# Kernel optimization log

Measured on AMD Instinct MI355X. Metric: run time of the kernel, lower is better.

Reference implementation:

```python
import jax, jax.numpy as jnp
import numpy as np

W_BIT = 8

def quantize_weight(w, k=W_BIT):
    # DoReFa-style weight quantization (conv2d_Q_fn): tanh-normalize to [0,1],
    # uniform-quantize to 2^k-1 levels (round with straight-through), map to [-1,1].
    n = float(2 ** k - 1)
    t = jnp.tanh(w)
    t = t / (2.0 * jnp.max(jnp.abs(t))) + 0.5
    q = t + jax.lax.stop_gradient(jnp.round(t * n) / n - t)
    return 2.0 * q - 1.0

def qconv(x, w, b, pad):
    wq = quantize_weight(w)
    y = jax.lax.conv_general_dilated(
        x, wq, window_strides=(1, 1), padding=[(pad, pad), (pad, pad)],
        dimension_numbers=('NCHW', 'OIHW', 'NCHW'))
    return y + b[None, :, None, None]

def upsample2x(x):
    # nearest-neighbor, scale_factor=2
    return jnp.repeat(jnp.repeat(x, 2, axis=2), 2, axis=3)

def setup_inputs() -> dict:
    key = jax.random.key(0)
    ks = jax.random.split(key, 11)
    F = 256
    C3 = jax.random.normal(ks[0], (8, 512, 64, 64), dtype=jnp.float32)
    C4 = jax.random.normal(ks[1], (8, 1024, 32, 32), dtype=jnp.float32)
    C5 = jax.random.normal(ks[2], (8, 2048, 16, 16), dtype=jnp.float32)
    # conv params (torch nn.Conv2d default has bias)
    w5 = jax.random.normal(ks[3], (F, 2048, 1, 1), dtype=jnp.float32) * 0.02
    b5 = jax.random.normal(ks[4], (F,), dtype=jnp.float32) * 0.01
    w4 = jax.random.normal(ks[5], (F, 1024, 1, 1), dtype=jnp.float32) * 0.02
    b4 = jax.random.normal(ks[6], (F,), dtype=jnp.float32) * 0.01
    w3 = jax.random.normal(ks[7], (F, 512, 1, 1), dtype=jnp.float32) * 0.02
    b3 = jax.random.normal(ks[8], (F,), dtype=jnp.float32) * 0.01
    w3_2 = jax.random.normal(ks[9], (F, F, 3, 3), dtype=jnp.float32) * 0.02
    b3_2 = jax.random.normal(ks[10], (F,), dtype=jnp.float32) * 0.01
    return {"C3": C3, "C4": C4, "C5": C5,
            "w5": w5, "b5": b5, "w4": w4, "b4": b4,
            "w3": w3, "b3": b3, "w3_2": w3_2, "b3_2": b3_2}

def reference(C3, C4, C5, w5, b5, w4, b4, w3, b3, w3_2, b3_2):
    P5_x = qconv(C5, w5, b5, pad=0)            # [B,256,16,16]
    P5_up = upsample2x(P5_x)                   # [B,256,32,32]
    P4_x = qconv(C4, w4, b4, pad=0) + P5_up    # [B,256,32,32]
    P4_up = upsample2x(P4_x)                   # [B,256,64,64]
    P3_x = qconv(C3, w3, b3, pad=0) + P4_up    # [B,256,64,64]
    P3_x = qconv(P3_x, w3_2, b3_2, pad=1)      # [B,256,64,64]
    return P3_x
```

## Files before the change

kernel.cpp:

```cpp
#include <hip/hip_runtime.h>
#include <stdint.h>

typedef unsigned short u16;
typedef short s16x8 __attribute__((ext_vector_type(8)));
typedef short s16x4 __attribute__((ext_vector_type(4)));
typedef float f32x4 __attribute__((ext_vector_type(4)));
typedef unsigned int u32x4 __attribute__((ext_vector_type(4)));

__device__ __forceinline__ u16 f2bf(float x) {
    unsigned u = __float_as_uint(x);
    unsigned r = u + 0x7FFFu + ((u >> 16) & 1u);
    return (u16)(r >> 16);
}

__device__ __forceinline__ void gll16(void* lds, const void* g) {
    __builtin_amdgcn_global_load_lds(
        (const __attribute__((address_space(1))) void*)g,
        (__attribute__((address_space(3))) void*)lds,
        16, 0, 0);
}

__global__ __launch_bounds__(256) void reduce_maxabs(
    const float* __restrict__ a0, int n0, const float* __restrict__ a1, int n1,
    const float* __restrict__ a2, int n2, const float* __restrict__ a3, int n3,
    float* __restrict__ out) {
    int which = blockIdx.y;
    const float* w = which == 0 ? a0 : which == 1 ? a1 : which == 2 ? a2 : a3;
    int n = which == 0 ? n0 : which == 1 ? n1 : which == 2 ? n2 : n3;
    float m = 0.f;
    for (int i = blockIdx.x * 256 + threadIdx.x; i < n; i += gridDim.x * 256)
        m = fmaxf(m, fabsf(tanhf(w[i])));
#pragma unroll
    for (int off = 32; off > 0; off >>= 1)
        m = fmaxf(m, __shfl_down(m, off, 64));
    __shared__ float sm[4];
    if ((threadIdx.x & 63) == 0) sm[threadIdx.x >> 6] = m;
    __syncthreads();
    if (threadIdx.x == 0) {
        m = fmaxf(fmaxf(sm[0], sm[1]), fmaxf(sm[2], sm[3]));
        atomicMax((int*)out + which, __float_as_int(m));
    }
}

__global__ __launch_bounds__(256) void quant_weights(
    const float* __restrict__ w5, const float* __restrict__ w4,
    const float* __restrict__ w3, const float* __restrict__ w32,
    const float* __restrict__ mx,
    u16* __restrict__ q5, u16* __restrict__ q4,
    u16* __restrict__ q3, u16* __restrict__ q2) {
    int which = blockIdx.y;
    const float* w = which == 0 ? w5 : which == 1 ? w4 : which == 2 ? w3 : w32;
    int n = which == 0 ? 524288 : which == 1 ? 262144 : which == 2 ? 131072 : 589824;
    int i = blockIdx.x * 256 + threadIdx.x;
    if (i >= n) return;
    float inv = 0.5f / mx[which];
    float t = tanhf(w[i]) * inv + 0.5f;
    float q = rintf(t * 255.f) * (1.f / 255.f);
    u16 o = f2bf(2.f * q - 1.f);
    if (which == 0) q5[i] = o;
    else if (which == 1) q4[i] = o;
    else if (which == 2) q3[i] = o;
    else {
        int kw = i % 3, kh = (i / 3) % 3, c = (i / 9) & 255, f = i / 2304;
        q2[(size_t)((kh * 3 + kw) * 256 + f) * 256 + c] = o;
    }
}

__global__ __launch_bounds__(256) void nchw_to_nhwc_bf16(
    const float* __restrict__ in, u16* __restrict__ outp, int C, int HW) {
    __shared__ float tile[64][65];
    int t = threadIdx.x;
    int hw0 = blockIdx.x << 6, c0 = blockIdx.y << 6, n = blockIdx.z;
    const float* src = in + (size_t)n * C * HW;
#pragma unroll
    for (int j = 0; j < 4; ++j) {
        int c = (t >> 4) + j * 16;
        int hw = (t & 15) << 2;
        f32x4 v = *(const f32x4*)(src + (size_t)(c0 + c) * HW + hw0 + hw);
        tile[c][hw] = v.x; tile[c][hw + 1] = v.y; tile[c][hw + 2] = v.z; tile[c][hw + 3] = v.w;
    }
    __syncthreads();
    u16* dst = outp + (size_t)n * C * HW;
#pragma unroll
    for (int j = 0; j < 16; ++j) {
        int idx = j * 256 + t;
        int c = idx & 63, hw = idx >> 6;
        dst[(size_t)(hw0 + hw) * C + c0 + c] = f2bf(tile[c][hw]);
    }
}

__global__ __launch_bounds__(256) void gemm_qconv(
    const u16* __restrict__ A, const u16* __restrict__ B,
    const float* __restrict__ bias, const float* __restrict__ addsrc,
    float* __restrict__ outF, u16* __restrict__ outB,
    int K, int Wlog, int HWlog) {
    __shared__ u16 As[128 * 64];
    __shared__ u16 Bs[128 * 64];
    int t = threadIdx.x, lane = t & 63, wv = t >> 6;
    int l16 = lane & 15, quad = lane >> 4;
    int f0 = blockIdx.y << 7, p0 = blockIdx.x << 7;
    int wf = (wv >> 1) << 6, wp = (wv & 1) << 6;
    f32x4 acc[4][4] = {};
    const u16* Ab = A + (size_t)f0 * K;
    const u16* Bb = B + (size_t)p0 * K;
    int row = t >> 3, c8 = t & 7;
    for (int k0 = 0; k0 < K; k0 += 64) {
#pragma unroll
        for (int it = 0; it < 4; ++it) {
            gll16(&As[(it * 256 + wv * 64) * 8], Ab + (size_t)(it * 32 + row) * K + k0 + c8 * 8);
            gll16(&Bs[(it * 256 + wv * 64) * 8], Bb + (size_t)(it * 32 + row) * K + k0 + c8 * 8);
        }
        __syncthreads();
#pragma unroll
        for (int kk = 0; kk < 64; kk += 32) {
            s16x8 a[4], b[4];
#pragma unroll
            for (int j = 0; j < 4; ++j)
                a[j] = *(const s16x8*)&As[(wf + 16 * j + l16) * 64 + kk + quad * 8];
#pragma unroll
            for (int i = 0; i < 4; ++i)
                b[i] = *(const s16x8*)&Bs[(wp + 16 * i + l16) * 64 + kk + quad * 8];
#pragma unroll
            for (int j = 0; j < 4; ++j)
#pragma unroll
                for (int i = 0; i < 4; ++i)
                    acc[j][i] = __builtin_amdgcn_mfma_f32_16x16x32_bf16(a[j], b[i], acc[j][i], 0, 0, 0);
        }
        __syncthreads();
    }
    int W = 1 << Wlog;
#pragma unroll
    for (int j = 0; j < 4; ++j) {
        int f = f0 + wf + 16 * j + (quad << 2);
        f32x4 bz = *(const f32x4*)(bias + f);
#pragma unroll
        for (int i = 0; i < 4; ++i) {
            int px = p0 + wp + 16 * i + l16;
            f32x4 v = acc[j][i] + bz;
            if (addsrc) {
                int n = px >> HWlog;
                int rem = px & ((1 << HWlog) - 1);
                int h = rem >> Wlog, ww = rem & (W - 1);
                int sp = (n << (HWlog - 2)) + ((h >> 1) << (Wlog - 1)) + (ww >> 1);
                v += *(const f32x4*)(addsrc + (size_t)sp * 256 + f);
            }
            if (outF) *(f32x4*)(outF + (size_t)px * 256 + f) = v;
            if (outB) {
                s16x4 o;
                o.x = (short)f2bf(v.x); o.y = (short)f2bf(v.y);
                o.z = (short)f2bf(v.z); o.w = (short)f2bf(v.w);
                *(s16x4*)(outB + (size_t)px * 256 + f) = o;
            }
        }
    }
}

#define CVS 40
__global__ __launch_bounds__(256) void conv3x3_q(
    const u16* __restrict__ X, const u16* __restrict__ Wq,
    const float* __restrict__ bias, float* __restrict__ outp) {
    __shared__ u16 Rg[6 * 66 * CVS];
    __shared__ u16 Aw[5 * 64 * CVS];
    int t = threadIdx.x, lane = t & 63, wv = t >> 6;
    int l16 = lane & 15, quad = lane >> 4;
    int n = blockIdx.x >> 4, h0 = (blockIdx.x & 15) << 2;
    int f0 = blockIdx.y << 6;
    f32x4 acc[4][4] = {};
    for (int c0 = 0; c0 < 256; c0 += 32) {
#pragma unroll
        for (int it = 0; it < 7; ++it) {
            int chunk = it * 256 + t;
            if (chunk < 1584) {
                int r = chunk / 264;
                int rest = chunk - r * 264;
                int w = rest >> 2, c8 = rest & 3;
                int h = h0 - 1 + r, ww = w - 1;
                u32x4 v; v.x = 0; v.y = 0; v.z = 0; v.w = 0;
                if ((unsigned)h < 64u && (unsigned)ww < 64u)
                    v = *(const u32x4*)(X + ((((size_t)n << 12) + (h << 6) + ww) << 8) + c0 + c8 * 8);
                *(u32x4*)(Rg + (r * 66 + w) * CVS + c8 * 8) = v;
            }
        }
#pragma unroll
        for (int it = 0; it < 5; ++it) {
            int chunk = it * 256 + t;
            int tap = chunk >> 8, fr = (chunk >> 2) & 63, cc = chunk & 3;
            *(u32x4*)(Aw + (tap * 64 + fr) * CVS + cc * 8) =
                *(const u32x4*)(Wq + (((size_t)tap * 256 + f0 + fr) << 8) + c0 + cc * 8);
        }
        __syncthreads();
#pragma unroll
        for (int tp = 0; tp < 5; ++tp) {
            int dh = tp / 3, dw = tp % 3;
            s16x8 a[4], b[4];
#pragma unroll
            for (int i = 0; i < 4; ++i)
                b[i] = *(const s16x8*)(Rg + ((wv + dh) * 66 + 16 * i + l16 + dw) * CVS + quad * 8);
#pragma unroll
            for (int j = 0; j < 4; ++j)
                a[j] = *(const s16x8*)(Aw + (tp * 64 + 16 * j + l16) * CVS + quad * 8);
#pragma unroll
            for (int j = 0; j < 4; ++j)
#pragma unroll
                for (int i = 0; i < 4; ++i)
                    acc[j][i] = __builtin_amdgcn_mfma_f32_16x16x32_bf16(a[j], b[i], acc[j][i], 0, 0, 0);
        }
        __syncthreads();
#pragma unroll
        for (int it = 0; it < 4; ++it) {
            int chunk = it * 256 + t;
            int tap = 5 + (chunk >> 8), fr = (chunk >> 2) & 63, cc = chunk & 3;
            *(u32x4*)(Aw + ((tap - 5) * 64 + fr) * CVS + cc * 8) =
                *(const u32x4*)(Wq + (((size_t)tap * 256 + f0 + fr) << 8) + c0 + cc * 8);
        }
        __syncthreads();
#pragma unroll
        for (int tp = 5; tp < 9; ++tp) {
            int dh = tp / 3, dw = tp % 3;
            s16x8 a[4], b[4];
#pragma unroll
            for (int i = 0; i < 4; ++i)
                b[i] = *(const s16x8*)(Rg + ((wv + dh) * 66 + 16 * i + l16 + dw) * CVS + quad * 8);
#pragma unroll
            for (int j = 0; j < 4; ++j)
                a[j] = *(const s16x8*)(Aw + ((tp - 5) * 64 + 16 * j + l16) * CVS + quad * 8);
#pragma unroll
            for (int j = 0; j < 4; ++j)
#pragma unroll
                for (int i = 0; i < 4; ++i)
                    acc[j][i] = __builtin_amdgcn_mfma_f32_16x16x32_bf16(a[j], b[i], acc[j][i], 0, 0, 0);
        }
        __syncthreads();
    }
    int h = h0 + wv;
#pragma unroll
    for (int j = 0; j < 4; ++j) {
        int f = f0 + 16 * j + (quad << 2);
        f32x4 bz = *(const f32x4*)(bias + f);
#pragma unroll
        for (int i = 0; i < 4; ++i) {
            int w = 16 * i + l16;
#pragma unroll
            for (int r = 0; r < 4; ++r)
                outp[((size_t)(n * 256 + f + r) << 12) + (h << 6) + w] = acc[j][i][r] + bz[r];
        }
    }
}

extern "C" void kernel_launch(void* const* d_in, const int* in_sizes, int n_in,
                              void* d_out, int out_size, void* d_ws, size_t ws_size,
                              hipStream_t stream) {
    (void)in_sizes; (void)n_in; (void)out_size; (void)ws_size;
    const float* C3  = (const float*)d_in[0];
    const float* C4  = (const float*)d_in[1];
    const float* C5  = (const float*)d_in[2];
    const float* w5  = (const float*)d_in[3];
    const float* b5  = (const float*)d_in[4];
    const float* w4  = (const float*)d_in[5];
    const float* b4  = (const float*)d_in[6];
    const float* w3  = (const float*)d_in[7];
    const float* b3  = (const float*)d_in[8];
    const float* w32 = (const float*)d_in[9];
    const float* b32 = (const float*)d_in[10];
    float* outp = (float*)d_out;

    char* p = (char*)d_ws;
    float* mx = (float*)p;  p += 256;
    u16* q5   = (u16*)p;    p += (size_t)524288 * 2;
    u16* q4   = (u16*)p;    p += (size_t)262144 * 2;
    u16* q3   = (u16*)p;    p += (size_t)131072 * 2;
    u16* q2   = (u16*)p;    p += (size_t)589824 * 2;
    u16* c5n  = (u16*)p;    p += (size_t)4194304 * 2;
    u16* c4n  = (u16*)p;    p += (size_t)8388608 * 2;
    u16* c3n  = (u16*)p;    p += (size_t)16777216 * 2;
    float* p5x = (float*)p; p += (size_t)2097152 * 4;
    float* p4x = (float*)p; p += (size_t)8388608 * 4;
    u16* p3xn = (u16*)p;    p += (size_t)8388608 * 2;

    hipMemsetAsync(d_ws, 0, 256, stream);
    reduce_maxabs<<<dim3(128, 4), 256, 0, stream>>>(w5, 524288, w4, 262144,
                                                    w3, 131072, w32, 589824, mx);
    quant_weights<<<dim3(2304, 4), 256, 0, stream>>>(w5, w4, w3, w32, mx, q5, q4, q3, q2);
    nchw_to_nhwc_bf16<<<dim3(4, 32, 8),  256, 0, stream>>>(C5, c5n, 2048, 256);
    nchw_to_nhwc_bf16<<<dim3(16, 16, 8), 256, 0, stream>>>(C4, c4n, 1024, 1024);
    nchw_to_nhwc_bf16<<<dim3(64, 8, 8),  256, 0, stream>>>(C3, c3n, 512, 4096);
    gemm_qconv<<<dim3(16, 2),  256, 0, stream>>>(q5, c5n, b5, nullptr, p5x, nullptr, 2048, 4, 8);
    gemm_qconv<<<dim3(64, 2),  256, 0, stream>>>(q4, c4n, b4, p5x, p4x, nullptr, 1024, 5, 10);
    gemm_qconv<<<dim3(256, 2), 256, 0, stream>>>(q3, c3n, b3, p4x, nullptr, p3xn, 512, 6, 12);
    conv3x3_q<<<dim3(128, 4), 256, 0, stream>>>(p3xn, q2, b32, outp);
}
```

Baseline: 330.1 us.

## Fuse prep kernels and split-K small GEMMs with templated tiles

Merges the weight quantization and the three NCHW-to-NHWC transposes into one launch and widens the transpose stores to 4-element vectors. The 1x1-conv GEMM becomes a template over tile size. The P5 GEMM now uses 64x64 tiles with split-K over two chunks, accumulating through atomics into a pre-zeroed buffer, and the P4 GEMM uses 64x128 tiles. The goal is more blocks on the small GEMMs, which previously launched only 32 and 128 workgroups, and fewer launches, at the cost of an extra memset and atomic traffic.

```diff
diff --git a/kernel.cpp b/kernel.cpp
--- a/kernel.cpp
+++ b/kernel.cpp
@@ -42,99 +42,125 @@
     }
 }
 
-__global__ __launch_bounds__(256) void quant_weights(
+__global__ __launch_bounds__(256) void prep(
     const float* __restrict__ w5, const float* __restrict__ w4,
     const float* __restrict__ w3, const float* __restrict__ w32,
     const float* __restrict__ mx,
     u16* __restrict__ q5, u16* __restrict__ q4,
-    u16* __restrict__ q3, u16* __restrict__ q2) {
-    int which = blockIdx.y;
-    const float* w = which == 0 ? w5 : which == 1 ? w4 : which == 2 ? w3 : w32;
-    int n = which == 0 ? 524288 : which == 1 ? 262144 : which == 2 ? 131072 : 589824;
-    int i = blockIdx.x * 256 + threadIdx.x;
-    if (i >= n) return;
-    float inv = 0.5f / mx[which];
-    float t = tanhf(w[i]) * inv + 0.5f;
-    float q = rintf(t * 255.f) * (1.f / 255.f);
-    u16 o = f2bf(2.f * q - 1.f);
-    if (which == 0) q5[i] = o;
-    else if (which == 1) q4[i] = o;
-    else if (which == 2) q3[i] = o;
-    else {
-        int kw = i % 3, kh = (i / 3) % 3, c = (i / 9) & 255, f = i / 2304;
-        q2[(size_t)((kh * 3 + kw) * 256 + f) * 256 + c] = o;
-    }
-}
-
-__global__ __launch_bounds__(256) void nchw_to_nhwc_bf16(
-    const float* __restrict__ in, u16* __restrict__ outp, int C, int HW) {
+    u16* __restrict__ q3, u16* __restrict__ q2,
+    const float* __restrict__ C5, const float* __restrict__ C4,
+    const float* __restrict__ C3,
+    u16* __restrict__ c5n, u16* __restrict__ c4n, u16* __restrict__ c3n) {
     __shared__ float tile[64][65];
     int t = threadIdx.x;
-    int hw0 = blockIdx.x << 6, c0 = blockIdx.y << 6, n = blockIdx.z;
-    const float* src = in + (size_t)n * C * HW;
+    int b = blockIdx.x;
+    if (b < 5888) {
+        int which, i;
+        const float* w;
+        if (b < 2048)      { which = 0; w = w5;  i = b * 256 + t; }
+        else if (b < 3072) { which = 1; w = w4;  i = (b - 2048) * 256 + t; }
+        else if (b < 3584) { which = 2; w = w3;  i = (b - 3072) * 256 + t; }
+        else               { which = 3; w = w32; i = (b - 3584) * 256 + t; }
+        float inv = 0.5f / mx[which];
+        float tt = tanhf(w[i]) * inv + 0.5f;
+        float q = rintf(tt * 255.f) * (1.f / 255.f);
+        u16 o = f2bf(2.f * q - 1.f);
+        if (which == 0) q5[i] = o;
+        else if (which == 1) q4[i] = o;
+        else if (which == 2) q3[i] = o;
+        else {
+            int kw = i % 3, kh = (i / 3) % 3, c = (i / 9) & 255, f = i / 2304;
+            q2[(size_t)((kh * 3 + kw) * 256 + f) * 256 + c] = o;
+        }
+        return;
+    }
+    b -= 5888;
+    const float* src; u16* dst; int C, HW, bx, by, nn;
+    if (b < 1024) {
+        nn = b >> 7; int r = b & 127; by = r >> 2; bx = r & 3;
+        C = 2048; HW = 256; src = C5; dst = c5n;
+    } else if (b < 3072) {
+        int l = b - 1024; nn = l >> 8; int r = l & 255; by = r >> 4; bx = r & 15;
+        C = 1024; HW = 1024; src = C4; dst = c4n;
+    } else {
+        int l = b - 3072; nn = l >> 9; int r = l & 511; by = r >> 6; bx = r & 63;
+        C = 512; HW = 4096; src = C3; dst = c3n;
+    }
+    int hw0 = bx << 6, c0 = by << 6;
+    const float* s2 = src + (size_t)nn * C * HW;
 #pragma unroll
     for (int j = 0; j < 4; ++j) {
         int c = (t >> 4) + j * 16;
         int hw = (t & 15) << 2;
-        f32x4 v = *(const f32x4*)(src + (size_t)(c0 + c) * HW + hw0 + hw);
+        f32x4 v = *(const f32x4*)(s2 + (size_t)(c0 + c) * HW + hw0 + hw);
         tile[c][hw] = v.x; tile[c][hw + 1] = v.y; tile[c][hw + 2] = v.z; tile[c][hw + 3] = v.w;
     }
     __syncthreads();
-    u16* dst = outp + (size_t)n * C * HW;
-#pragma unroll
-    for (int j = 0; j < 16; ++j) {
+    u16* d2 = dst + (size_t)nn * C * HW;
+#pragma unroll
+    for (int j = 0; j < 4; ++j) {
         int idx = j * 256 + t;
-        int c = idx & 63, hw = idx >> 6;
-        dst[(size_t)(hw0 + hw) * C + c0 + c] = f2bf(tile[c][hw]);
-    }
-}
-
+        int c4 = (idx & 15) << 2, hw = idx >> 4;
+        s16x4 o;
+        o.x = (short)f2bf(tile[c4][hw]);
+        o.y = (short)f2bf(tile[c4 + 1][hw]);
+        o.z = (short)f2bf(tile[c4 + 2][hw]);
+        o.w = (short)f2bf(tile[c4 + 3][hw]);
+        *(s16x4*)(d2 + (size_t)(hw0 + hw) * C + c0 + c4) = o;
+    }
+}
+
+template<int BF, int BPX, int FJ, int FI>
 __global__ __launch_bounds__(256) void gemm_qconv(
     const u16* __restrict__ A, const u16* __restrict__ B,
     const float* __restrict__ bias, const float* __restrict__ addsrc,
     float* __restrict__ outF, u16* __restrict__ outB,
-    int K, int Wlog, int HWlog) {
-    __shared__ u16 As[128 * 64];
-    __shared__ u16 Bs[128 * 64];
+    int Kfull, int Kchunk, int Wlog, int HWlog, int atomic_out) {
+    __shared__ u16 As[BF * 64];
+    __shared__ u16 Bs[BPX * 64];
     int t = threadIdx.x, lane = t & 63, wv = t >> 6;
     int l16 = lane & 15, quad = lane >> 4;
-    int f0 = blockIdx.y << 7, p0 = blockIdx.x << 7;
-    int wf = (wv >> 1) << 6, wp = (wv & 1) << 6;
-    f32x4 acc[4][4] = {};
-    const u16* Ab = A + (size_t)f0 * K;
-    const u16* Bb = B + (size_t)p0 * K;
+    int f0 = blockIdx.y * BF, p0 = blockIdx.x * BPX;
+    int wf = (wv >> 1) * (BF / 2), wp = (wv & 1) * (BPX / 2);
+    f32x4 acc[FJ][FI] = {};
+    const u16* Ab = A + (size_t)f0 * Kfull;
+    const u16* Bb = B + (size_t)p0 * Kfull;
     int row = t >> 3, c8 = t & 7;
-    for (int k0 = 0; k0 < K; k0 += 64) {
-#pragma unroll
-        for (int it = 0; it < 4; ++it) {
-            gll16(&As[(it * 256 + wv * 64) * 8], Ab + (size_t)(it * 32 + row) * K + k0 + c8 * 8);
-            gll16(&Bs[(it * 256 + wv * 64) * 8], Bb + (size_t)(it * 32 + row) * K + k0 + c8 * 8);
-        }
+    int k_begin = blockIdx.z * Kchunk, k_end = k_begin + Kchunk;
+    for (int k0 = k_begin; k0 < k_end; k0 += 64) {
+#pragma unroll
+        for (int it = 0; it < BF / 32; ++it)
+            gll16(&As[(it * 256 + wv * 64) * 8], Ab + (size_t)(it * 32 + row) * Kfull + k0 + c8 * 8);
+#pragma unroll
+        for (int it = 0; it < BPX / 32; ++it)
+            gll16(&Bs[(it * 256 + wv * 64) * 8], Bb + (size_t)(it * 32 + row) * Kfull + k0 + c8 * 8);
         __syncthreads();
 #pragma unroll
         for (int kk = 0; kk < 64; kk += 32) {
-            s16x8 a[4], b[4];
-#pragma unroll
-            for (int j = 0; j < 4; ++j)
+            s16x8 a[FJ], b[FI];
+#pragma unroll
+            for (int j = 0; j < FJ; ++j)
                 a[j] = *(const s16x8*)&As[(wf + 16 * j + l16) * 64 + kk + quad * 8];
 #pragma unroll
-            for (int i = 0; i < 4; ++i)
+            for (int i = 0; i < FI; ++i)
                 b[i] = *(const s16x8*)&Bs[(wp + 16 * i + l16) * 64 + kk + quad * 8];
 #pragma unroll
-            for (int j = 0; j < 4; ++j)
-#pragma unroll
-                for (int i = 0; i < 4; ++i)
+            for (int j = 0; j < FJ; ++j)
+#pragma unroll
+                for (int i = 0; i < FI; ++i)
                     acc[j][i] = __builtin_amdgcn_mfma_f32_16x16x32_bf16(a[j], b[i], acc[j][i], 0, 0, 0);
         }
         __syncthreads();
     }
     int W = 1 << Wlog;
-#pragma unroll
-    for (int j = 0; j < 4; ++j) {
+    bool bias_on = (blockIdx.z == 0);
+#pragma unroll
+    for (int j = 0; j < FJ; ++j) {
         int f = f0 + wf + 16 * j + (quad << 2);
-        f32x4 bz = *(const f32x4*)(bias + f);
-#pragma unroll
-        for (int i = 0; i < 4; ++i) {
+        f32x4 bz = {0.f, 0.f, 0.f, 0.f};
+        if (bias_on) bz = *(const f32x4*)(bias + f);
+#pragma unroll
+        for (int i = 0; i < FI; ++i) {
             int px = p0 + wp + 16 * i + l16;
             f32x4 v = acc[j][i] + bz;
             if (addsrc) {
@@ -144,12 +170,17 @@
                 int sp = (n << (HWlog - 2)) + ((h >> 1) << (Wlog - 1)) + (ww >> 1);
                 v += *(const f32x4*)(addsrc + (size_t)sp * 256 + f);
             }
-            if (outF) *(f32x4*)(outF + (size_t)px * 256 + f) = v;
-            if (outB) {
+            if (atomic_out) {
+                float* d = outF + (size_t)px * 256 + f;
+                atomicAdd(d + 0, v.x); atomicAdd(d + 1, v.y);
+                atomicAdd(d + 2, v.z); atomicAdd(d + 3, v.w);
+            } else if (outB) {
                 s16x4 o;
                 o.x = (short)f2bf(v.x); o.y = (short)f2bf(v.y);
                 o.z = (short)f2bf(v.z); o.w = (short)f2bf(v.w);
                 *(s16x4*)(outB + (size_t)px * 256 + f) = o;
+            } else {
+                *(f32x4*)(outF + (size_t)px * 256 + f) = v;
             }
         }
     }
@@ -277,15 +308,17 @@
     float* p4x = (float*)p; p += (size_t)8388608 * 4;
     u16* p3xn = (u16*)p;    p += (size_t)8388608 * 2;
 
-    hipMemsetAsync(d_ws, 0, 256, stream);
+    hipMemsetAsync(mx, 0, 256, stream);
+    hipMemsetAsync(p5x, 0, (size_t)2097152 * 4, stream);
     reduce_maxabs<<<dim3(128, 4), 256, 0, stream>>>(w5, 524288, w4, 262144,
                                                     w3, 131072, w32, 589824, mx);
-    quant_weights<<<dim3(2304, 4), 256, 0, stream>>>(w5, w4, w3, w32, mx, q5, q4, q3, q2);
-    nchw_to_nhwc_bf16<<<dim3(4, 32, 8),  256, 0, stream>>>(C5, c5n, 2048, 256);
-    nchw_to_nhwc_bf16<<<dim3(16, 16, 8), 256, 0, stream>>>(C4, c4n, 1024, 1024);
-    nchw_to_nhwc_bf16<<<dim3(64, 8, 8),  256, 0, stream>>>(C3, c3n, 512, 4096);
-    gemm_qconv<<<dim3(16, 2),  256, 0, stream>>>(q5, c5n, b5, nullptr, p5x, nullptr, 2048, 4, 8);
-    gemm_qconv<<<dim3(64, 2),  256, 0, stream>>>(q4, c4n, b4, p5x, p4x, nullptr, 1024, 5, 10);
-    gemm_qconv<<<dim3(256, 2), 256, 0, stream>>>(q3, c3n, b3, p4x, nullptr, p3xn, 512, 6, 12);
+    prep<<<13056, 256, 0, stream>>>(w5, w4, w3, w32, mx, q5, q4, q3, q2,
+                                    C5, C4, C3, c5n, c4n, c3n);
+    gemm_qconv<64, 64, 2, 2><<<dim3(32, 4, 2), 256, 0, stream>>>(
+        q5, c5n, b5, nullptr, p5x, nullptr, 2048, 1024, 4, 8, 1);
+    gemm_qconv<64, 128, 2, 4><<<dim3(64, 4, 1), 256, 0, stream>>>(
+        q4, c4n, b4, p5x, p4x, nullptr, 1024, 1024, 5, 10, 0);
+    gemm_qconv<128, 128, 4, 4><<<dim3(256, 2, 1), 256, 0, stream>>>(
+        q3, c3n, b3, p4x, nullptr, p3xn, 512, 512, 6, 12, 0);
     conv3x3_q<<<dim3(128, 4), 256, 0, stream>>>(p3xn, q2, b32, outp);
 }
```

Result: faster. 305.6 us (-7.4%).
